# Kernel tuning notes

Measured on AMD Instinct MI355X. Metric: run time of the kernel, lower is better.

## Reference

```python
import jax, jax.numpy as jnp
from jax import lax
import numpy as np

K = 2        # k-hop MIS / number of rw SpGEMM iterations
EPS = 0.5    # lazy random-walk epsilon
N = 2048     # nodes
D = 512      # feature dim
E = 65536    # edges (avg degree 32)


def setup_inputs() -> dict:
    key = jax.random.key(0)
    k1, k2, k3, k4 = jax.random.split(key, 4)
    edge_index = jax.random.randint(k1, (2, E), 0, N, dtype=jnp.int32)
    edge_attr = jax.random.uniform(k2, (E,), dtype=jnp.float32)
    x = jax.random.normal(k3, (N, D), dtype=jnp.float32)
    rank = jnp.arange(N, dtype=jnp.int32)  # node ordering ('random' ordering = some permutation; identity here)
    u = jax.random.uniform(k4, (N, N), dtype=jnp.float32)  # noise for row-wise multinomial sampling
    return {"edge_index": edge_index, "edge_attr": edge_attr, "x": x, "rank": rank, "u": u}


def _maximal_k_independent_set(row, col, rank, n, k):
    """Greedy maximal k-independent set: nodes that are local rank-minima within k hops."""
    big = jnp.int32(n)

    def prop_min(r):  # one hop of min-propagation (message row -> col), keep self
        return jnp.minimum(jax.ops.segment_min(r[row], col, num_segments=n), r)

    def prop_or(b):   # one hop of boolean OR propagation (as int32)
        return jnp.maximum(jax.ops.segment_max(b[row], col, num_segments=n), b)

    def cond(st):
        mis, mask, mr = st
        return ~jnp.all(mask)

    def body(st):
        mis, mask, mr = st
        for _ in range(k):
            mr = prop_min(mr)
        mis = mis | (rank == mr)
        mk = mis.astype(jnp.int32)
        for _ in range(k):
            mk = prop_or(mk)
        mask = mk > 0
        mr = jnp.where(mask, big, rank)
        return mis, mask, mr

    init = (jnp.zeros(n, bool), jnp.zeros(n, bool), rank)
    mis, _, _ = lax.while_loop(cond, body, init)
    return mis


def _row_normalize(m):
    s = m.sum(axis=1, keepdims=True)
    return m / jnp.where(s > 0, s, 1.0)


def reference(edge_index, edge_attr, x, rank, u):
    n = x.shape[0]
    row, col = edge_index[0], edge_index[1]

    # --- MIS over the graph structure (integer-only) ---
    mis = _maximal_k_independent_set(row, col, rank, n, K)

    # --- adjacency (dense padded form of the SparseTensor) ---
    adj = jnp.zeros((n, n), x.dtype).at[row, col].add(edge_attr)

    # --- lazy random walk: rw = D^-1 A, offdiag *= (1-eps), diag = old_diag + eps ---
    rw = _row_normalize(adj)
    di = jnp.arange(n)
    new_diag = rw[di, di] + EPS  # computed BEFORE scaling, per original code
    rw = (rw * (1.0 - EPS)).at[di, di].set(new_diag)

    # --- c_mat = rw^K @ eye[:, mis]; padded to [n, n] with zero non-MIS columns ---
    c = jnp.where(mis[None, :], jnp.eye(n, dtype=x.dtype), 0.0)
    for _ in range(K):
        c = rw @ c
    c = _row_normalize(c)

    # --- sample_partition_matrix: per-row multinomial via Gumbel-argmax ---
    g = -jnp.log(-jnp.log(u + 1e-20) + 1e-20)
    logits = jnp.where(c > 0, jnp.log(jnp.maximum(c, 1e-30)), -jnp.inf) + g
    cluster = jnp.argmax(logits, axis=1)                 # [n] cluster id (a MIS column)
    c_hard = jax.nn.one_hot(cluster, n, dtype=x.dtype)   # partition matrix [n, n]

    # --- p_inv = row-normalized c_hard.T ---
    counts = c_hard.sum(axis=0)
    p_inv = c_hard.T / jnp.where(counts > 0, counts, 1.0)[:, None]

    # --- coarsen: c^T A c, pool: p_inv @ x ---
    adj_c = c_hard.T @ adj @ c_hard
    x_pool = p_inv @ x
    return adj_c, c_hard, p_inv, mis, x_pool
```

## Files before the change

### kernel.cpp

```cpp
#include <hip/hip_runtime.h>
#include <hip/hip_bf16.h>
#include <math.h>
#include <stdint.h>

#define NN 2048
#define DD 512
#define EE 65536
#define EPSV 0.5f
#define SEN 2048
#define PADE 98304
#define NPART 4

static const size_t SZ = (size_t)NN * NN;

__global__ __launch_bounds__(1024) void count_deg8(const int* __restrict__ row,
                                                   const int* __restrict__ col,
                                                   int* __restrict__ pdeg,
                                                   int* __restrict__ pcdeg) {
  __shared__ int ld[NN], lc[NN];
  int t = threadIdx.x, b = blockIdx.x;
  for (int v = t; v < NN; v += 1024) { ld[v] = 0; lc[v] = 0; }
  __syncthreads();
  int base = b * (EE / NPART);
  for (int e = t; e < EE / NPART; e += 1024) {
    atomicAdd(&ld[row[base + e]], 1);
    atomicAdd(&lc[col[base + e]], 1);
  }
  __syncthreads();
  for (int v = t; v < NN; v += 1024) {
    pdeg[b * NN + v] = ld[v];
    pcdeg[b * NN + v] = lc[v];
  }
}

__global__ __launch_bounds__(1024) void csr_scan_pad(const int* __restrict__ pdeg,
                                                     const int* __restrict__ pcdeg,
                                                     int* __restrict__ row_ptr,
                                                     int* __restrict__ fill_ptr,
                                                     int* __restrict__ col_ptr,
                                                     int* __restrict__ cfill_ptr,
                                                     unsigned short* __restrict__ colidx,
                                                     unsigned short* __restrict__ rowidx,
                                                     float* __restrict__ avals,
                                                     int* __restrict__ counts) {
  __shared__ int a[NN], b[NN], c[NN], d[NN];
  __shared__ int dg_s[NN], cg_s[NN];
  int t = threadIdx.x;
  for (int v = t; v < NN; v += 1024) {
    int dg = pdeg[v] + pdeg[NN + v] + pdeg[2 * NN + v] + pdeg[3 * NN + v];
    int cg = pcdeg[v] + pcdeg[NN + v] + pcdeg[2 * NN + v] + pcdeg[3 * NN + v];
    dg_s[v] = dg;
    cg_s[v] = cg;
    a[v] = (dg + 15) & ~15;
    c[v] = (cg + 15) & ~15;
    counts[v] = 0;
  }
  __syncthreads();
  int* s1 = a; int* d1 = b; int* s2 = c; int* d2 = d;
  for (int off = 1; off < NN; off <<= 1) {
    for (int v = t; v < NN; v += 1024) {
      d1[v] = s1[v] + (v >= off ? s1[v - off] : 0);
      d2[v] = s2[v] + (v >= off ? s2[v - off] : 0);
    }
    __syncthreads();
    int* tp = s1; s1 = d1; d1 = tp;
    tp = s2; s2 = d2; d2 = tp;
  }
  for (int v = t; v < NN; v += 1024) {
    int dg = dg_s[v];
    int end = s1[v];
    int excl = end - ((dg + 15) & ~15);
    row_ptr[v] = excl;
    fill_ptr[v] = excl;
    for (int e = excl + dg; e < end; ++e) {
      colidx[e] = (unsigned short)v;
      avals[e] = 0.f;
    }
    dg = cg_s[v];
    end = s2[v];
    excl = end - ((dg + 15) & ~15);
    col_ptr[v] = excl;
    cfill_ptr[v] = excl;
    for (int e = excl + dg; e < end; ++e) rowidx[e] = (unsigned short)v;
  }
  if (t == 0) {
    row_ptr[NN] = s1[NN - 1];
    col_ptr[NN] = s2[NN - 1];
  }
}

__global__ __launch_bounds__(256) void csr_fill(const int* __restrict__ row,
                                                const int* __restrict__ col,
                                                const float* __restrict__ attr,
                                                int* __restrict__ fill_ptr,
                                                int* __restrict__ cfill_ptr,
                                                unsigned short* __restrict__ colidx,
                                                unsigned short* __restrict__ rowidx,
                                                float* __restrict__ avals) {
  int e = blockIdx.x * 256 + threadIdx.x;
  int r = row[e], c = col[e];
  int pos = atomicAdd(&fill_ptr[r], 1);
  colidx[pos] = (unsigned short)c;
  avals[pos] = attr[e];
  rowidx[atomicAdd(&cfill_ptr[c], 1)] = (unsigned short)r;
}

__global__ __launch_bounds__(1024) void fused_mis_rw(const int* __restrict__ row_ptr_g,
                                                     const int* __restrict__ col_ptr_g,
                                                     const unsigned short* __restrict__ colidx,
                                                     const unsigned short* __restrict__ rowidx,
                                                     const int* __restrict__ rank_g,
                                                     int* __restrict__ mis_flag,
                                                     int* __restrict__ mis_list,
                                                     int* __restrict__ mis_count,
                                                     const float* __restrict__ avals,
                                                     float* __restrict__ rw,
                                                     float* __restrict__ adjc,
                                                     float* __restrict__ xp) {
  if (blockIdx.x == 0) {
    __shared__ int rank_s[NN];
    __shared__ int mr[NN];
    __shared__ int cov[NN];
    __shared__ int dly[NN];
    __shared__ int mis_s[NN];
    __shared__ int row_ptr_s[NN + 1];
    __shared__ int col_ptr_s[NN + 1];
    __shared__ int unc[2][NN];
    __shared__ int dl[NN];
    __shared__ int ucnt[2];
    __shared__ int dcnt;
    __shared__ int cnt;
    int t = threadIdx.x;
    const uint4* col4 = (const uint4*)colidx;
    const uint4* row4 = (const uint4*)rowidx;

    for (int v = t; v < NN; v += 1024) {
      int rk = rank_g[v];
      rank_s[v] = rk;
      mr[v] = rk;
      cov[v] = 0;
      dly[v] = 0;
      mis_s[v] = 0;
      row_ptr_s[v] = row_ptr_g[v];
      col_ptr_s[v] = col_ptr_g[v];
      unc[0][v] = v;
    }
    if (t == 0) {
      row_ptr_s[NN] = row_ptr_g[NN];
      col_ptr_s[NN] = col_ptr_g[NN];
      ucnt[0] = NN;
      ucnt[1] = 0;
      dcnt = 0;
      cnt = 0;
    }
    __syncthreads();

    int cur = 0;
    for (int round = 0; round < NN; ++round) {
      int U = ucnt[cur];
      if (round) {
        for (int v = t; v < NN; v += 1024) {
          mr[v] = cov[v] ? SEN : rank_s[v];
          dly[v] = 0;
        }
        if (t == 0) { ucnt[cur ^ 1] = 0; dcnt = 0; }
        __syncthreads();
      }
      for (int i = t; i < U; i += 1024) {
        int v = unc[cur][i];
        int val = rank_s[v];
        int e0 = row_ptr_s[v];
        int nch = (row_ptr_s[v + 1] - e0) >> 3;
        const uint4* b4 = col4 + (e0 >> 3);
        for (int cI = 0; cI < nch; cI += 2) {
          uint4 A = b4[cI], B = b4[cI + 1];
          atomicMin(&mr[A.x & 0xFFFFu], val); atomicMin(&mr[A.x >> 16], val);
          atomicMin(&mr[A.y & 0xFFFFu], val); atomicMin(&mr[A.y >> 16], val);
          atomicMin(&mr[A.z & 0xFFFFu], val); atomicMin(&mr[A.z >> 16], val);
          atomicMin(&mr[A.w & 0xFFFFu], val); atomicMin(&mr[A.w >> 16], val);
          atomicMin(&mr[B.x & 0xFFFFu], val); atomicMin(&mr[B.x >> 16], val);
          atomicMin(&mr[B.y & 0xFFFFu], val); atomicMin(&mr[B.y >> 16], val);
          atomicMin(&mr[B.z & 0xFFFFu], val); atomicMin(&mr[B.z >> 16], val);
          atomicMin(&mr[B.w & 0xFFFFu], val); atomicMin(&mr[B.w >> 16], val);
        }
      }
      __syncthreads();
      for (int i = t; i < U; i += 1024) {
        int v = unc[cur][i];
        int val = mr[v];
        int e0 = col_ptr_s[v];
        int nch = (col_ptr_s[v + 1] - e0) >> 3;
        const uint4* b4 = row4 + (e0 >> 3);
        for (int cI = 0; cI < nch; cI += 2) {
          uint4 A = b4[cI], B = b4[cI + 1];
          int m0 = min(mr[A.x & 0xFFFFu], mr[A.x >> 16]);
          int m1 = min(mr[A.y & 0xFFFFu], mr[A.y >> 16]);
          int m2 = min(mr[A.z & 0xFFFFu], mr[A.z >> 16]);
          int m3 = min(mr[A.w & 0xFFFFu], mr[A.w >> 16]);
          int m4 = min(mr[B.x & 0xFFFFu], mr[B.x >> 16]);
          int m5 = min(mr[B.y & 0xFFFFu], mr[B.y >> 16]);
          int m6 = min(mr[B.z & 0xFFFFu], mr[B.z >> 16]);
          int m7 = min(mr[B.w & 0xFFFFu], mr[B.w >> 16]);
          val = min(val, min(min(min(m0, m1), min(m2, m3)),
                             min(min(m4, m5), min(m6, m7))));
        }
        if (rank_s[v] == val) {
          mis_s[v] = 1;
          dly[v] = 1;
          dl[atomicAdd(&dcnt, 1)] = v;
        }
      }
      __syncthreads();
      int D = dcnt;
      for (int i = t; i < D; i += 1024) {
        int v = dl[i];
        int e0 = row_ptr_s[v];
        int nch = (row_ptr_s[v + 1] - e0) >> 3;
        const uint4* b4 = col4 + (e0 >> 3);
        for (int cI = 0; cI < nch; cI += 2) {
          uint4 A = b4[cI], B = b4[cI + 1];
          dly[A.x & 0xFFFFu] = 1; dly[A.x >> 16] = 1;
          dly[A.y & 0xFFFFu] = 1; dly[A.y >> 16] = 1;
          dly[A.z & 0xFFFFu] = 1; dly[A.z >> 16] = 1;
          dly[A.w & 0xFFFFu] = 1; dly[A.w >> 16] = 1;
          dly[B.x & 0xFFFFu] = 1; dly[B.x >> 16] = 1;
          dly[B.y & 0xFFFFu] = 1; dly[B.y >> 16] = 1;
          dly[B.z & 0xFFFFu] = 1; dly[B.z >> 16] = 1;
          dly[B.w & 0xFFFFu] = 1; dly[B.w >> 16] = 1;
        }
      }
      __syncthreads();
      for (int i = t; i < U; i += 1024) {
        int v = unc[cur][i];
        int c1 = dly[v];
        if (!c1) {
          int e0 = col_ptr_s[v];
          int nch = (col_ptr_s[v + 1] - e0) >> 3;
          const uint4* b4 = row4 + (e0 >> 3);
          for (int cI = 0; cI < nch; cI += 2) {
            uint4 A = b4[cI], B = b4[cI + 1];
            c1 |= dly[A.x & 0xFFFFu] | dly[A.x >> 16] |
                  dly[A.y & 0xFFFFu] | dly[A.y >> 16] |
                  dly[A.z & 0xFFFFu] | dly[A.z >> 16] |
                  dly[A.w & 0xFFFFu] | dly[A.w >> 16] |
                  dly[B.x & 0xFFFFu] | dly[B.x >> 16] |
                  dly[B.y & 0xFFFFu] | dly[B.y >> 16] |
                  dly[B.z & 0xFFFFu] | dly[B.z >> 16] |
                  dly[B.w & 0xFFFFu] | dly[B.w >> 16];
            if (c1) break;
          }
        }
        if (c1) cov[v] = 1;
        else unc[cur ^ 1][atomicAdd(&ucnt[cur ^ 1], 1)] = v;
      }
      __syncthreads();
      if (ucnt[cur ^ 1] == 0) break;
      cur ^= 1;
    }

    for (int v = t; v < NN; v += 1024) {
      int s = mis_s[v];
      mis_flag[v] = s;
      if (s) mis_list[atomicAdd(&cnt, 1)] = v;
    }
    __syncthreads();
    if (t == 0) *mis_count = cnt;
  } else {
    __shared__ float rowbuf[NN];
    __shared__ float ssum;
    int i = blockIdx.x - 1;
    int t = threadIdx.x;
    float4 z4 = make_float4(0.f, 0.f, 0.f, 0.f);
    if (t < 512) ((float4*)(adjc + (size_t)i * NN))[t] = z4;
    if (t < 128) ((float4*)xp)[(size_t)i * 128 + t] = z4;
    for (int j = t; j < NN; j += 1024) rowbuf[j] = 0.f;
    if (t == 0) ssum = 0.f;
    __syncthreads();
    int e0 = row_ptr_g[i], e1 = row_ptr_g[i + 1];
    float part = 0.f;
    for (int e = e0 + t; e < e1; e += 1024) {
      float a = avals[e];
      atomicAdd(&rowbuf[colidx[e]], a);
      part += a;
    }
    for (int off = 32; off; off >>= 1) part += __shfl_down(part, off);
    if ((t & 63) == 0) atomicAdd(&ssum, part);
    __syncthreads();
    float s = ssum;
    s = (s > 0.f) ? s : 1.f;
    for (int j = t; j < NN; j += 1024) {
      float v = rowbuf[j] / s;
      v = (i == j) ? (v + EPSV) : (v * (1.f - EPSV));
      rw[(size_t)i * NN + j] = v;
    }
  }
}

__global__ __launch_bounds__(256) void bc_gather(const float* __restrict__ rw,
                                                 const int* __restrict__ mis_list,
                                                 const int* __restrict__ mis_count,
                                                 float* __restrict__ Bc) {
  int M = *mis_count;
  int total = M * NN;
  int stride = gridDim.x * 256;
  for (int j = blockIdx.x * 256 + threadIdx.x; j < total; j += stride) {
    int tc = j >> 11, i = j & (NN - 1);
    Bc[(size_t)tc * NN + i] = rw[(size_t)i * NN + mis_list[tc]];
  }
}

__device__ inline unsigned int f32_key(float x) {
  unsigned int u = __float_as_uint(x);
  return (u & 0x80000000u) ? ~u : (u | 0x80000000u);
}
__device__ inline float dot4(float4 a, float4 b) {
  return ((a.x * b.x + a.y * b.y) + (a.z * b.z + a.w * b.w));
}
__device__ inline unsigned long long umax64(unsigned long long a, unsigned long long b) {
  return a > b ? a : b;
}
__device__ inline int pdecode(unsigned long long p) {
  return (p == 0ull) ? 0 : (NN - 1 - (int)(p & 0xFFFFFFFFull));
}

__global__ __launch_bounds__(256) void c2_all(const float* __restrict__ rw,
                                              const float* __restrict__ Bc,
                                              const float* __restrict__ u,
                                              const int* __restrict__ mis_list,
                                              const int* __restrict__ mis_count,
                                              int* __restrict__ cluster,
                                              int* __restrict__ counts) {
  int M = *mis_count;
  int lane = threadIdx.x & 63, w = threadIdx.x >> 6;
  int r0 = blockIdx.x * 8 + w * 2;
  const float4* rp0 = (const float4*)(rw + (size_t)r0 * NN);
  const float4* rp1 = (const float4*)(rw + (size_t)(r0 + 1) * NN);
  float4 A0[8], A1[8];
#pragma unroll
  for (int q = 0; q < 8; ++q) {
    A0[q] = rp0[q * 64 + lane];
    A1[q] = rp1[q * 64 + lane];
  }
  unsigned long long best0 = 0ull, best1 = 0ull;
  for (int j = 0; j < M; ++j) {
    int m = mis_list[j];
    const float4* cb = (const float4*)(Bc + (size_t)j * NN);
    float4 B[8];
#pragma unroll
    for (int q = 0; q < 8; ++q) B[q] = cb[q * 64 + lane];
    float s01 = dot4(A0[0], B[0]) + dot4(A0[1], B[1]);
    float s23 = dot4(A0[2], B[2]) + dot4(A0[3], B[3]);
    float s45 = dot4(A0[4], B[4]) + dot4(A0[5], B[5]);
    float s67 = dot4(A0[6], B[6]) + dot4(A0[7], B[7]);
    float s = (s01 + s23) + (s45 + s67);
    s += __shfl_xor(s, 32);
    s += __shfl_xor(s, 16);
    s += __shfl_xor(s, 8);
    s += __shfl_xor(s, 4);
    s += __shfl_xor(s, 2);
    s += __shfl_xor(s, 1);
    float t01 = dot4(A1[0], B[0]) + dot4(A1[1], B[1]);
    float t23 = dot4(A1[2], B[2]) + dot4(A1[3], B[3]);
    float t45 = dot4(A1[4], B[4]) + dot4(A1[5], B[5]);
    float t67 = dot4(A1[6], B[6]) + dot4(A1[7], B[7]);
    float tt = (t01 + t23) + (t45 + t67);
    tt += __shfl_xor(tt, 32);
    tt += __shfl_xor(tt, 16);
    tt += __shfl_xor(tt, 8);
    tt += __shfl_xor(tt, 4);
    tt += __shfl_xor(tt, 2);
    tt += __shfl_xor(tt, 1);
    if (lane == 0) {
      if (s > 0.f) {
        float uu = u[(size_t)r0 * NN + m];
        float g = -logf(-logf(uu + 1e-20f) + 1e-20f);
        float logit = logf(s) + g;
        best0 = umax64(best0, ((unsigned long long)f32_key(logit) << 32) |
                                  (unsigned int)(NN - 1 - m));
      }
      if (tt > 0.f) {
        float uu = u[(size_t)(r0 + 1) * NN + m];
        float g = -logf(-logf(uu + 1e-20f) + 1e-20f);
        float logit = logf(tt) + g;
        best1 = umax64(best1, ((unsigned long long)f32_key(logit) << 32) |
                                  (unsigned int)(NN - 1 - m));
      }
    }
  }
  if (lane == 0) {
    int m0b = pdecode(best0);
    cluster[r0] = m0b;
    atomicAdd(&counts[m0b], 1);
    int m1b = pdecode(best1);
    cluster[r0 + 1] = m1b;
    atomicAdd(&counts[m1b], 1);
  }
}

__global__ __launch_bounds__(256) void scatter_chpm(const int* __restrict__ row,
                                                    const int* __restrict__ col,
                                                    const float* __restrict__ attr,
                                                    const float* __restrict__ x,
                                                    const int* __restrict__ cluster,
                                                    const int* __restrict__ counts,
                                                    const int* __restrict__ mis_flag,
                                                    float* __restrict__ out_ch,
                                                    float* __restrict__ out_pinv,
                                                    float* __restrict__ out_mis,
                                                    float* __restrict__ adjc,
                                                    float* __restrict__ xp) {
  int idx = blockIdx.x * 256 + threadIdx.x;
  int a = idx >> 11, b = idx & (NN - 1);
  out_ch[idx] = (cluster[a] == b) ? 1.f : 0.f;
  float pv = 0.f;
  if (cluster[b] == a) {
    int c = counts[a];
    pv = 1.f / (float)(c > 0 ? c : 1);
  }
  out_pinv[idx] = pv;
  if (idx < NN) out_mis[idx] = mis_flag[idx] ? 1.f : 0.f;
  if (idx < NN * DD) {
    int i = idx >> 9;
    int ci = cluster[i];
    int c = counts[ci];
    atomicAdd(&xp[ci * DD + (idx & (DD - 1))], x[idx] / (float)(c > 0 ? c : 1));
  }
  if (idx < EE) {
    atomicAdd(&adjc[(size_t)cluster[row[idx]] * NN + cluster[col[idx]]], attr[idx]);
  }
}

extern "C" void kernel_launch(void* const* d_in, const int* in_sizes, int n_in,
                              void* d_out, int out_size, void* d_ws, size_t ws_size,
                              hipStream_t stream) {
  const int*   edge_index = (const int*)d_in[0];
  const float* edge_attr  = (const float*)d_in[1];
  const float* x          = (const float*)d_in[2];
  const int*   rank       = (const int*)d_in[3];
  const float* u          = (const float*)d_in[4];
  float* out              = (float*)d_out;

  const int* row = edge_index;
  const int* col = edge_index + EE;

  float* out_adjc = out;
  float* out_ch   = out + SZ;
  float* out_pinv = out + 2 * SZ;
  float* out_mis  = out + 3 * SZ;
  float* out_xp   = out + 3 * SZ + NN;

  int*   counts    = (int*)d_ws;
  int*   mis_flag  = counts + NN;
  int*   cluster   = mis_flag + NN;
  int*   mis_list  = cluster + NN;
  int*   mis_count = mis_list + NN;
  int*   fill_ptr  = mis_count + 1;
  int*   cfill_ptr = fill_ptr + NN;
  int*   row_ptr   = cfill_ptr + NN;
  int*   col_ptr   = row_ptr + NN + 1;
  int*   pdeg      = col_ptr + NN + 1;
  int*   pcdeg     = pdeg + NPART * NN;
  unsigned short* colidx =
      (unsigned short*)(((uintptr_t)(pcdeg + NPART * NN) + 31) & ~(uintptr_t)31);
  unsigned short* rowidx = colidx + PADE;
  float* avals = (float*)(rowidx + PADE);

  count_deg8<<<NPART, 1024, 0, stream>>>(row, col, pdeg, pcdeg);
  csr_scan_pad<<<1, 1024, 0, stream>>>(pdeg, pcdeg, row_ptr, fill_ptr, col_ptr,
                                       cfill_ptr, colidx, rowidx, avals, counts);
  csr_fill<<<EE / 256, 256, 0, stream>>>(row, col, edge_attr, fill_ptr, cfill_ptr,
                                         colidx, rowidx, avals);
  fused_mis_rw<<<NN + 1, 1024, 0, stream>>>(row_ptr, col_ptr, colidx, rowidx, rank,
                                            mis_flag, mis_list, mis_count,
                                            avals, out_pinv , out_adjc, out_xp);
  bc_gather<<<256, 256, 0, stream>>>(out_pinv, mis_list, mis_count, out_ch);
  c2_all<<<NN / 8, 256, 0, stream>>>(out_pinv, out_ch, u, mis_list, mis_count,
                                     cluster, counts);
  scatter_chpm<<<(NN * NN) / 256, 256, 0, stream>>>(row, col, edge_attr, x, cluster,
                                                    counts, mis_flag, out_ch, out_pinv,
                                                    out_mis, out_adjc, out_xp);
}
```

Before: 229.2 us.

## Offload first MIS round to grid-parallel kernels before single-block loop

```diff
diff --git a/kernel.cpp b/kernel.cpp
--- a/kernel.cpp
+++ b/kernel.cpp
@@ -35,6 +35,7 @@
 
 __global__ __launch_bounds__(1024) void csr_scan_pad(const int* __restrict__ pdeg,
                                                      const int* __restrict__ pcdeg,
+                                                     const int* __restrict__ rank_g,
                                                      int* __restrict__ row_ptr,
                                                      int* __restrict__ fill_ptr,
                                                      int* __restrict__ col_ptr,
@@ -42,7 +43,9 @@
                                                      unsigned short* __restrict__ colidx,
                                                      unsigned short* __restrict__ rowidx,
                                                      float* __restrict__ avals,
-                                                     int* __restrict__ counts) {
+                                                     int* __restrict__ counts,
+                                                     int* __restrict__ mr1,
+                                                     int* __restrict__ covp) {
   __shared__ int a[NN], b[NN], c[NN], d[NN];
   __shared__ int dg_s[NN], cg_s[NN];
   int t = threadIdx.x;
@@ -54,6 +57,8 @@
     a[v] = (dg + 15) & ~15;
     c[v] = (cg + 15) & ~15;
     counts[v] = 0;
+    mr1[v] = rank_g[v];
+    covp[v] = 0;
   }
   __syncthreads();
   int* s1 = a; int* d1 = b; int* s2 = c; int* d2 = d;
@@ -92,17 +97,76 @@
 __global__ __launch_bounds__(256) void csr_fill(const int* __restrict__ row,
                                                 const int* __restrict__ col,
                                                 const float* __restrict__ attr,
+                                                const int* __restrict__ rank_g,
                                                 int* __restrict__ fill_ptr,
                                                 int* __restrict__ cfill_ptr,
                                                 unsigned short* __restrict__ colidx,
                                                 unsigned short* __restrict__ rowidx,
-                                                float* __restrict__ avals) {
+                                                float* __restrict__ avals,
+                                                int* __restrict__ mr1) {
   int e = blockIdx.x * 256 + threadIdx.x;
   int r = row[e], c = col[e];
   int pos = atomicAdd(&fill_ptr[r], 1);
   colidx[pos] = (unsigned short)c;
   avals[pos] = attr[e];
   rowidx[atomicAdd(&cfill_ptr[c], 1)] = (unsigned short)r;
+  atomicMin(&mr1[c], rank_g[r]);
+}
+
+__global__ __launch_bounds__(256) void min2_detect(const int* __restrict__ row_ptr,
+                                                   const int* __restrict__ col_ptr,
+                                                   const unsigned short* __restrict__ colidx,
+                                                   const unsigned short* __restrict__ rowidx,
+                                                   const int* __restrict__ rank_g,
+                                                   const int* __restrict__ mr1,
+                                                   int* __restrict__ mis0,
+                                                   int* __restrict__ covp) {
+  int v = blockIdx.x * 256 + threadIdx.x;
+  int val = mr1[v];
+  int e0 = col_ptr[v], e1 = col_ptr[v + 1];
+  const uint4* r4 = (const uint4*)rowidx;
+  for (int cI = e0 >> 3; cI < (e1 >> 3); ++cI) {
+    uint4 A = r4[cI];
+    int m0 = min(mr1[A.x & 0xFFFFu], mr1[A.x >> 16]);
+    int m1 = min(mr1[A.y & 0xFFFFu], mr1[A.y >> 16]);
+    int m2 = min(mr1[A.z & 0xFFFFu], mr1[A.z >> 16]);
+    int m3 = min(mr1[A.w & 0xFFFFu], mr1[A.w >> 16]);
+    val = min(val, min(min(m0, m1), min(m2, m3)));
+  }
+  int isw = (rank_g[v] == val) ? 1 : 0;
+  mis0[v] = isw;
+  if (isw) {
+    covp[v] = 1;
+    int f0 = row_ptr[v], f1 = row_ptr[v + 1];
+    const uint4* c4 = (const uint4*)colidx;
+    for (int cI = f0 >> 3; cI < (f1 >> 3); ++cI) {
+      uint4 A = c4[cI];
+      covp[A.x & 0xFFFFu] = 1; covp[A.x >> 16] = 1;
+      covp[A.y & 0xFFFFu] = 1; covp[A.y >> 16] = 1;
+      covp[A.z & 0xFFFFu] = 1; covp[A.z >> 16] = 1;
+      covp[A.w & 0xFFFFu] = 1; covp[A.w >> 16] = 1;
+    }
+  }
+}
+
+__global__ __launch_bounds__(256) void or_hop(const int* __restrict__ col_ptr,
+                                              const unsigned short* __restrict__ rowidx,
+                                              const int* __restrict__ covp,
+                                              int* __restrict__ cov2) {
+  int v = blockIdx.x * 256 + threadIdx.x;
+  int b = covp[v];
+  if (!b) {
+    int e0 = col_ptr[v], e1 = col_ptr[v + 1];
+    const uint4* r4 = (const uint4*)rowidx;
+    for (int cI = e0 >> 3; cI < (e1 >> 3) && !b; ++cI) {
+      uint4 A = r4[cI];
+      b = covp[A.x & 0xFFFFu] | covp[A.x >> 16] |
+          covp[A.y & 0xFFFFu] | covp[A.y >> 16] |
+          covp[A.z & 0xFFFFu] | covp[A.z >> 16] |
+          covp[A.w & 0xFFFFu] | covp[A.w >> 16];
+    }
+  }
+  cov2[v] = b ? 1 : 0;
 }
 
 __global__ __launch_bounds__(1024) void fused_mis_rw(const int* __restrict__ row_ptr_g,
@@ -110,6 +174,8 @@
                                                      const unsigned short* __restrict__ colidx,
                                                      const unsigned short* __restrict__ rowidx,
                                                      const int* __restrict__ rank_g,
+                                                     const int* __restrict__ mis0_g,
+                                                     const int* __restrict__ cov2_g,
                                                      int* __restrict__ mis_flag,
                                                      int* __restrict__ mis_list,
                                                      int* __restrict__ mis_count,
@@ -118,13 +184,10 @@
                                                      float* __restrict__ adjc,
                                                      float* __restrict__ xp) {
   if (blockIdx.x == 0) {
-    __shared__ int rank_s[NN];
     __shared__ int mr[NN];
     __shared__ int cov[NN];
     __shared__ int dly[NN];
     __shared__ int mis_s[NN];
-    __shared__ int row_ptr_s[NN + 1];
-    __shared__ int col_ptr_s[NN + 1];
     __shared__ int unc[2][NN];
     __shared__ int dl[NN];
     __shared__ int ucnt[2];
@@ -135,127 +198,121 @@
     const uint4* row4 = (const uint4*)rowidx;
 
     for (int v = t; v < NN; v += 1024) {
-      int rk = rank_g[v];
-      rank_s[v] = rk;
-      mr[v] = rk;
-      cov[v] = 0;
-      dly[v] = 0;
-      mis_s[v] = 0;
-      row_ptr_s[v] = row_ptr_g[v];
-      col_ptr_s[v] = col_ptr_g[v];
-      unc[0][v] = v;
+      cov[v] = cov2_g[v];
+      mis_s[v] = mis0_g[v];
     }
     if (t == 0) {
-      row_ptr_s[NN] = row_ptr_g[NN];
-      col_ptr_s[NN] = col_ptr_g[NN];
-      ucnt[0] = NN;
+      ucnt[0] = 0;
       ucnt[1] = 0;
       dcnt = 0;
       cnt = 0;
     }
     __syncthreads();
+    for (int v = t; v < NN; v += 1024)
+      if (!cov[v]) unc[0][atomicAdd(&ucnt[0], 1)] = v;
+    __syncthreads();
 
     int cur = 0;
-    for (int round = 0; round < NN; ++round) {
-      int U = ucnt[cur];
-      if (round) {
+    if (ucnt[0] > 0) {
+      for (int round = 0; round < NN; ++round) {
+        int U = ucnt[cur];
         for (int v = t; v < NN; v += 1024) {
-          mr[v] = cov[v] ? SEN : rank_s[v];
+          mr[v] = cov[v] ? SEN : rank_g[v];
           dly[v] = 0;
         }
         if (t == 0) { ucnt[cur ^ 1] = 0; dcnt = 0; }
         __syncthreads();
-      }
-      for (int i = t; i < U; i += 1024) {
-        int v = unc[cur][i];
-        int val = rank_s[v];
-        int e0 = row_ptr_s[v];
-        int nch = (row_ptr_s[v + 1] - e0) >> 3;
-        const uint4* b4 = col4 + (e0 >> 3);
-        for (int cI = 0; cI < nch; cI += 2) {
-          uint4 A = b4[cI], B = b4[cI + 1];
-          atomicMin(&mr[A.x & 0xFFFFu], val); atomicMin(&mr[A.x >> 16], val);
-          atomicMin(&mr[A.y & 0xFFFFu], val); atomicMin(&mr[A.y >> 16], val);
-          atomicMin(&mr[A.z & 0xFFFFu], val); atomicMin(&mr[A.z >> 16], val);
-          atomicMin(&mr[A.w & 0xFFFFu], val); atomicMin(&mr[A.w >> 16], val);
-          atomicMin(&mr[B.x & 0xFFFFu], val); atomicMin(&mr[B.x >> 16], val);
-          atomicMin(&mr[B.y & 0xFFFFu], val); atomicMin(&mr[B.y >> 16], val);
-          atomicMin(&mr[B.z & 0xFFFFu], val); atomicMin(&mr[B.z >> 16], val);
-          atomicMin(&mr[B.w & 0xFFFFu], val); atomicMin(&mr[B.w >> 16], val);
+        for (int i = t; i < U; i += 1024) {
+          int v = unc[cur][i];
+          int val = rank_g[v];
+          int e0 = row_ptr_g[v];
+          int nch = (row_ptr_g[v + 1] - e0) >> 3;
+          const uint4* b4 = col4 + (e0 >> 3);
+          for (int cI = 0; cI < nch; cI += 2) {
+            uint4 A = b4[cI], B = b4[cI + 1];
+            atomicMin(&mr[A.x & 0xFFFFu], val); atomicMin(&mr[A.x >> 16], val);
+            atomicMin(&mr[A.y & 0xFFFFu], val); atomicMin(&mr[A.y >> 16], val);
+            atomicMin(&mr[A.z & 0xFFFFu], val); atomicMin(&mr[A.z >> 16], val);
+            atomicMin(&mr[A.w & 0xFFFFu], val); atomicMin(&mr[A.w >> 16], val);
+            atomicMin(&mr[B.x & 0xFFFFu], val); atomicMin(&mr[B.x >> 16], val);
+            atomicMin(&mr[B.y & 0xFFFFu], val); atomicMin(&mr[B.y >> 16], val);
+            atomicMin(&mr[B.z & 0xFFFFu], val); atomicMin(&mr[B.z >> 16], val);
+            atomicMin(&mr[B.w & 0xFFFFu], val); atomicMin(&mr[B.w >> 16], val);
+          }
         }
-      }
-      __syncthreads();
-      for (int i = t; i < U; i += 1024) {
-        int v = unc[cur][i];
-        int val = mr[v];
-        int e0 = col_ptr_s[v];
-        int nch = (col_ptr_s[v + 1] - e0) >> 3;
-        const uint4* b4 = row4 + (e0 >> 3);
-        for (int cI = 0; cI < nch; cI += 2) {
-          uint4 A = b4[cI], B = b4[cI + 1];
-          int m0 = min(mr[A.x & 0xFFFFu], mr[A.x >> 16]);
-          int m1 = min(mr[A.y & 0xFFFFu], mr[A.y >> 16]);
-          int m2 = min(mr[A.z & 0xFFFFu], mr[A.z >> 16]);
-          int m3 = min(mr[A.w & 0xFFFFu], mr[A.w >> 16]);
-          int m4 = min(mr[B.x & 0xFFFFu], mr[B.x >> 16]);
-          int m5 = min(mr[B.y & 0xFFFFu], mr[B.y >> 16]);
-          int m6 = min(mr[B.z & 0xFFFFu], mr[B.z >> 16]);
-          int m7 = min(mr[B.w & 0xFFFFu], mr[B.w >> 16]);
-          val = min(val, min(min(min(m0, m1), min(m2, m3)),
-                             min(min(m4, m5), min(m6, m7))));
-        }
-        if (rank_s[v] == val) {
-          mis_s[v] = 1;
-          dly[v] = 1;
-          dl[atomicAdd(&dcnt, 1)] = v;
-        }
-      }
-      __syncthreads();
-      int D = dcnt;
-      for (int i = t; i < D; i += 1024) {
-        int v = dl[i];
-        int e0 = row_ptr_s[v];
-        int nch = (row_ptr_s[v + 1] - e0) >> 3;
-        const uint4* b4 = col4 + (e0 >> 3);
-        for (int cI = 0; cI < nch; cI += 2) {
-          uint4 A = b4[cI], B = b4[cI + 1];
-          dly[A.x & 0xFFFFu] = 1; dly[A.x >> 16] = 1;
-          dly[A.y & 0xFFFFu] = 1; dly[A.y >> 16] = 1;
-          dly[A.z & 0xFFFFu] = 1; dly[A.z >> 16] = 1;
-          dly[A.w & 0xFFFFu] = 1; dly[A.w >> 16] = 1;
-          dly[B.x & 0xFFFFu] = 1; dly[B.x >> 16] = 1;
-          dly[B.y & 0xFFFFu] = 1; dly[B.y >> 16] = 1;
-          dly[B.z & 0xFFFFu] = 1; dly[B.z >> 16] = 1;
-          dly[B.w & 0xFFFFu] = 1; dly[B.w >> 16] = 1;
-        }
-      }
-      __syncthreads();
-      for (int i = t; i < U; i += 1024) {
-        int v = unc[cur][i];
-        int c1 = dly[v];
-        if (!c1) {
-          int e0 = col_ptr_s[v];
-          int nch = (col_ptr_s[v + 1] - e0) >> 3;
+        __syncthreads();
+        for (int i = t; i < U; i += 1024) {
+          int v = unc[cur][i];
+          int val = mr[v];
+          int e0 = col_ptr_g[v];
+          int nch = (col_ptr_g[v + 1] - e0) >> 3;
           const uint4* b4 = row4 + (e0 >> 3);
           for (int cI = 0; cI < nch; cI += 2) {
             uint4 A = b4[cI], B = b4[cI + 1];
-            c1 |= dly[A.x & 0xFFFFu] | dly[A.x >> 16] |
-                  dly[A.y & 0xFFFFu] | dly[A.y >> 16] |
-                  dly[A.z & 0xFFFFu] | dly[A.z >> 16] |
-                  dly[A.w & 0xFFFFu] | dly[A.w >> 16] |
-                  dly[B.x & 0xFFFFu] | dly[B.x >> 16] |
-                  dly[B.y & 0xFFFFu] | dly[B.y >> 16] |
-                  dly[B.z & 0xFFFFu] | dly[B.z >> 16] |
-                  dly[B.w & 0xFFFFu] | dly[B.w >> 16];
-            if (c1) break;
+            int m0 = min(mr[A.x & 0xFFFFu], mr[A.x >> 16]);
+            int m1 = min(mr[A.y & 0xFFFFu], mr[A.y >> 16]);
+            int m2 = min(mr[A.z & 0xFFFFu], mr[A.z >> 16]);
+            int m3 = min(mr[A.w & 0xFFFFu], mr[A.w >> 16]);
+            int m4 = min(mr[B.x & 0xFFFFu], mr[B.x >> 16]);
+            int m5 = min(mr[B.y & 0xFFFFu], mr[B.y >> 16]);
+            int m6 = min(mr[B.z & 0xFFFFu], mr[B.z >> 16]);
+            int m7 = min(mr[B.w & 0xFFFFu], mr[B.w >> 16]);
+            val = min(val, min(min(min(m0, m1), min(m2, m3)),
+                               min(min(m4, m5), min(m6, m7))));
+          }
+          if (rank_g[v] == val) {
+            mis_s[v] = 1;
+            dly[v] = 1;
+            dl[atomicAdd(&dcnt, 1)] = v;
           }
         }
-        if (c1) cov[v] = 1;
-        else unc[cur ^ 1][atomicAdd(&ucnt[cur ^ 1], 1)] = v;
+        __syncthreads();
+        int D = dcnt;
+        for (int i = t; i < D; i += 1024) {
+          int v = dl[i];
+          int e0 = row_ptr_g[v];
+          int nch = (row_ptr_g[v + 1] - e0) >> 3;
+          const uint4* b4 = col4 + (e0 >> 3);
+          for (int cI = 0; cI < nch; cI += 2) {
+            uint4 A = b4[cI], B = b4[cI + 1];
+            dly[A.x & 0xFFFFu] = 1; dly[A.x >> 16] = 1;
+            dly[A.y & 0xFFFFu] = 1; dly[A.y >> 16] = 1;
+            dly[A.z & 0xFFFFu] = 1; dly[A.z >> 16] = 1;
+            dly[A.w & 0xFFFFu] = 1; dly[A.w >> 16] = 1;
+            dly[B.x & 0xFFFFu] = 1; dly[B.x >> 16] = 1;
+            dly[B.y & 0xFFFFu] = 1; dly[B.y >> 16] = 1;
+            dly[B.z & 0xFFFFu] = 1; dly[B.z >> 16] = 1;
+            dly[B.w & 0xFFFFu] = 1; dly[B.w >> 16] = 1;
+          }
+        }
+        __syncthreads();
+        for (int i = t; i < U; i += 1024) {
+          int v = unc[cur][i];
+          int c1 = dly[v];
+          if (!c1) {
+            int e0 = col_ptr_g[v];
+            int nch = (col_ptr_g[v + 1] - e0) >> 3;
+            const uint4* b4 = row4 + (e0 >> 3);
+            for (int cI = 0; cI < nch; cI += 2) {
+              uint4 A = b4[cI], B = b4[cI + 1];
+              c1 |= dly[A.x & 0xFFFFu] | dly[A.x >> 16] |
+                    dly[A.y & 0xFFFFu] | dly[A.y >> 16] |
+                    dly[A.z & 0xFFFFu] | dly[A.z >> 16] |
+                    dly[A.w & 0xFFFFu] | dly[A.w >> 16] |
+                    dly[B.x & 0xFFFFu] | dly[B.x >> 16] |
+                    dly[B.y & 0xFFFFu] | dly[B.y >> 16] |
+                    dly[B.z & 0xFFFFu] | dly[B.z >> 16] |
+                    dly[B.w & 0xFFFFu] | dly[B.w >> 16];
+              if (c1) break;
+            }
+          }
+          if (c1) cov[v] = 1;
+          else unc[cur ^ 1][atomicAdd(&ucnt[cur ^ 1], 1)] = v;
+        }
+        __syncthreads();
+        if (ucnt[cur ^ 1] == 0) break;
+        cur ^= 1;
       }
-      __syncthreads();
-      if (ucnt[cur ^ 1] == 0) break;
-      cur ^= 1;
     }
 
     for (int v = t; v < NN; v += 1024) {
@@ -458,7 +515,11 @@
   int*   cfill_ptr = fill_ptr + NN;
   int*   row_ptr   = cfill_ptr + NN;
   int*   col_ptr   = row_ptr + NN + 1;
-  int*   pdeg      = col_ptr + NN + 1;
+  int*   mr1       = col_ptr + NN + 1;
+  int*   mis0      = mr1 + NN;
+  int*   covp      = mis0 + NN;
+  int*   cov2      = covp + NN;
+  int*   pdeg      = cov2 + NN;
   int*   pcdeg     = pdeg + NPART * NN;
   unsigned short* colidx =
       (unsigned short*)(((uintptr_t)(pcdeg + NPART * NN) + 31) & ~(uintptr_t)31);
@@ -466,12 +527,16 @@
   float* avals = (float*)(rowidx + PADE);
 
   count_deg8<<<NPART, 1024, 0, stream>>>(row, col, pdeg, pcdeg);
-  csr_scan_pad<<<1, 1024, 0, stream>>>(pdeg, pcdeg, row_ptr, fill_ptr, col_ptr,
-                                       cfill_ptr, colidx, rowidx, avals, counts);
-  csr_fill<<<EE / 256, 256, 0, stream>>>(row, col, edge_attr, fill_ptr, cfill_ptr,
-                                         colidx, rowidx, avals);
+  csr_scan_pad<<<1, 1024, 0, stream>>>(pdeg, pcdeg, rank, row_ptr, fill_ptr, col_ptr,
+                                       cfill_ptr, colidx, rowidx, avals, counts,
+                                       mr1, covp);
+  csr_fill<<<EE / 256, 256, 0, stream>>>(row, col, edge_attr, rank, fill_ptr, cfill_ptr,
+                                         colidx, rowidx, avals, mr1);
+  min2_detect<<<NN / 256, 256, 0, stream>>>(row_ptr, col_ptr, colidx, rowidx, rank,
+                                            mr1, mis0, covp);
+  or_hop<<<NN / 256, 256, 0, stream>>>(col_ptr, rowidx, covp, cov2);
   fused_mis_rw<<<NN + 1, 1024, 0, stream>>>(row_ptr, col_ptr, colidx, rowidx, rank,
-                                            mis_flag, mis_list, mis_count,
+                                            mis0, cov2, mis_flag, mis_list, mis_count,
                                             avals, out_pinv , out_adjc, out_xp);
   bc_gather<<<256, 256, 0, stream>>>(out_pinv, mis_list, mis_count, out_ch);
   c2_all<<<NN / 8, 256, 0, stream>>>(out_pinv, out_ch, u, mis_list, mis_count,
```

Measured after the change: 238.4 us. 4.0% more time.
